# Kernel optimization log

Hardware: AMD Instinct MI355X
Metric: run time of the kernel (lower is better)

Reference implementation:

```python
import jax, jax.numpy as jnp
import numpy as np

# Static DAG: input -> L hidden layers of K nodes (dense between layers) -> output.
B, WIDTH, K, L = 262144, 64, 4, 4


def _linear_init(key, shape, fan_in):
    # matches nn.Linear default: U(-1/sqrt(fan_in), 1/sqrt(fan_in))
    bound = 1.0 / np.sqrt(fan_in)
    return jax.random.uniform(key, shape, jnp.float32, -bound, bound)


def setup_inputs() -> dict:
    key = jax.random.key(0)
    ks = jax.random.split(key, 9)
    x = jax.random.normal(ks[0], (B, WIDTH), jnp.float32)
    # input node -> first hidden layer (K edges)
    W_in = _linear_init(ks[1], (K, WIDTH, WIDTH), WIDTH)
    b_in = _linear_init(ks[2], (K, WIDTH), WIDTH)
    # between hidden layers: (L-1) transitions, K*K edges each; [pred, node, out, in]
    W_mid = _linear_init(ks[3], (L - 1, K, K, WIDTH, WIDTH), WIDTH)
    b_mid = _linear_init(ks[4], (L - 1, K, K, WIDTH), WIDTH)
    # last hidden layer -> output node (K edges)
    W_out = _linear_init(ks[5], (K, WIDTH, WIDTH), WIDTH)
    b_out = _linear_init(ks[6], (K, WIDTH), WIDTH)
    return {"x": x, "W_in": W_in, "b_in": b_in, "W_mid": W_mid,
            "b_mid": b_mid, "W_out": W_out, "b_out": b_out}


def _l2_normalize(t):
    # torch.linalg.norm(t) with no dim: Frobenius norm over the WHOLE tensor
    return t / jnp.linalg.norm(t)


def reference(x, W_in, b_in, W_mid, b_mid, W_out, b_out):
    # input node -> layer 1: each node k gets a single edge Linear, then normalize
    h = jnp.einsum('bw,kvw->kbv', x, W_in) + b_in[:, None, :]  # [K,B,W]
    h = jax.vmap(_l2_normalize)(h)
    # hidden -> hidden transitions: node v sums over its K predecessor edges
    for l in range(L - 1):  # small fixed structural loop over layers
        pre = jnp.einsum('pbw,pkvw->kbv', h, W_mid[l]) + b_mid[l].sum(axis=0)[:, None, :]
        h = jax.vmap(_l2_normalize)(pre)
    # last layer -> output node: sum K edge outputs, normalize
    out = jnp.einsum('pbw,pvw->bv', h, W_out) + b_out.sum(axis=0)
    return _l2_normalize(out)
```

## Files before the change

### kernel.cpp

```cpp
#include <hip/hip_runtime.h>


#define BF 262144.0f

#define OFF_G   0
#define OFF_S   4096
#define OFF_P0  8192
#define OFF_P1  73728
#define OFF_C0  139264
#define OFF_C1  140288
#define OFF_MO  141312
#define OFF_CO  145408

typedef __attribute__((ext_vector_type(8))) short bf16x8;
typedef __attribute__((ext_vector_type(4))) float f32x4;

__device__ __forceinline__ unsigned short f2bf(float f) {
  unsigned u = __builtin_bit_cast(unsigned, f);
  u += 0x7FFF + ((u >> 16) & 1);
  return (unsigned short)(u >> 16);
}
__device__ __forceinline__ float bf2f(unsigned short h) {
  unsigned u = ((unsigned)h) << 16;
  return __builtin_bit_cast(float, u);
}

__device__ __forceinline__ bf16x8 cvt8(f32x4 a, f32x4 b, float s) {
  bf16x8 t;
#pragma unroll
  for (int j = 0; j < 4; j++) {
    t[j]     = (short)f2bf(a[j] * s);
    t[j + 4] = (short)f2bf(b[j] * s);
  }
  return t;
}

__global__ __launch_bounds__(256) void kG(const float* __restrict__ x,
                                          float* __restrict__ Gpart) {
  __shared__ __align__(16) unsigned short xts[4][4][16][8];
  __shared__ float sred[256][4];
  const int tid = threadIdx.x;
  const int lane = tid & 63, mt = tid >> 6;
  const int col = lane & 15, q = lane >> 4;
  const int row0 = tid >> 4;
  const int cf0  = (tid & 15) * 4;

  f32x4 acc[4];
#pragma unroll
  for (int nt = 0; nt < 4; nt++) acc[nt] = (f32x4){0.f, 0.f, 0.f, 0.f};
  float s0 = 0.f, s1 = 0.f, s2 = 0.f, s3 = 0.f;

  const float* bx = x + (long)blockIdx.x * 32768;
  f32x4 r0 = *(const f32x4*)(bx + tid * 4);
  f32x4 r1 = *(const f32x4*)(bx + 1024 + tid * 4);

  for (int c = 0; c < 16; c++) {
    __syncthreads();
    s0 += r0[0] + r1[0]; s1 += r0[1] + r1[1];
    s2 += r0[2] + r1[2]; s3 += r0[3] + r1[3];
#pragma unroll
    for (int j = 0; j < 4; j++) {
      const int cf = cf0 + j;
      xts[cf >> 4][row0 >> 3][cf & 15][row0 & 7]        = f2bf(r0[j]);
      xts[cf >> 4][2 + (row0 >> 3)][cf & 15][row0 & 7]  = f2bf(r1[j]);
    }
    f32x4 r0n = r0, r1n = r1;
    if (c < 15) {
      r0n = *(const f32x4*)(bx + (c + 1) * 2048 + tid * 4);
      r1n = *(const f32x4*)(bx + (c + 1) * 2048 + 1024 + tid * 4);
    }
    __syncthreads();
    const bf16x8 af = *(const bf16x8*)xts[mt][q][col];
#pragma unroll
    for (int nt = 0; nt < 4; nt++) {
      const bf16x8 bfr = *(const bf16x8*)xts[nt][q][col];
      acc[nt] = __builtin_amdgcn_mfma_f32_16x16x32_bf16(af, bfr, acc[nt], 0, 0, 0);
    }
    r0 = r0n; r1 = r1n;
  }

  float* myp = Gpart + (long)blockIdx.x * 4160;
#pragma unroll
  for (int nt = 0; nt < 4; nt++)
#pragma unroll
    for (int r = 0; r < 4; r++)
      myp[(mt * 16 + q * 4 + r) * 64 + nt * 16 + col] = acc[nt][r];

  sred[tid][0] = s0; sred[tid][1] = s1; sred[tid][2] = s2; sred[tid][3] = s3;
  __syncthreads();
  if (tid < 64) {
    float t = 0.f;
#pragma unroll
    for (int k2 = 0; k2 < 16; k2++) t += sred[(tid >> 2) + 16 * k2][tid & 3];
    myp[4096 + tid] = t;
  }
}

__global__ __launch_bounds__(256) void kGred(const float* __restrict__ Gpart,
                                             float* __restrict__ G,
                                             float* __restrict__ s) {
  __shared__ float red[4][64];
  const int tid = threadIdx.x;
  const int e = blockIdx.x * 64 + (tid & 63);
  const int quarter = tid >> 6;
  float acc = 0.f;
#pragma unroll 4
  for (int j = 0; j < 128; j++)
    acc += Gpart[(long)(quarter * 128 + j) * 4160 + e];
  red[quarter][tid & 63] = acc;
  __syncthreads();
  if (tid < 64) {
    const float t = red[0][tid] + red[1][tid] + red[2][tid] + red[3][tid];
    const int ee = blockIdx.x * 64 + tid;
    if (ee < 4096) G[ee] = t;
    else           s[ee - 4096] = t;
  }
}

__global__ __launch_bounds__(256) void kLayer(const float* __restrict__ Tsrc,
                                              const float* __restrict__ csrc,
                                              const float* __restrict__ Wm,
                                              const float* __restrict__ bm,
                                              const float* __restrict__ G,
                                              const float* __restrict__ s,
                                              float* __restrict__ Pout,
                                              float* __restrict__ cpout,
                                              const int KN, const int first) {
  __shared__ float Tf[64][68];
  __shared__ __align__(16) unsigned short Tth[64][68], Ttl[64][68];
  __shared__ __align__(16) unsigned short Wh[64][68], Wlo[64][68];
  __shared__ float red[256];
  __shared__ __align__(16) float cl[64], sl[64];
  const int tid = threadIdx.x;
  const int p = blockIdx.x / KN, kk = blockIdx.x % KN;
  const int lane = tid & 63, it = tid >> 6;
  const int col = lane & 15, quad = lane >> 4;

  float Greg[4][4];
#pragma unroll
  for (int ut = 0; ut < 4; ut++)
#pragma unroll
    for (int r = 0; r < 4; r++)
      Greg[ut][r] = G[(it * 16 + quad * 4 + r) * 64 + ut * 16 + col];

#pragma unroll
  for (int m = 0; m < 16; m++) {
    const int li = m * 256 + tid;
    const int r = li >> 6, cc = li & 63;
    float tv;
    if (first) tv = Tsrc[p * 4096 + li];
    else tv = Tsrc[p * 4096 + li] + Tsrc[(4 + p) * 4096 + li] +
              Tsrc[(8 + p) * 4096 + li] + Tsrc[(12 + p) * 4096 + li];
    Tf[r][cc] = tv;
    const float wv = Wm[(long)(p * KN + kk) * 4096 + li];
    const unsigned short wh = f2bf(wv);
    Wh[r][cc] = wh;
    Wlo[r][cc] = f2bf(wv - bf2f(wh));
  }
  if (tid < 64) {
    float cv;
    if (first) cv = csrc[p * 64 + tid];
    else cv = csrc[p * 64 + tid] + csrc[(4 + p) * 64 + tid] +
              csrc[(8 + p) * 64 + tid] + csrc[(12 + p) * 64 + tid];
    cl[tid] = cv;
    sl[tid] = s[tid];
  }
  __syncthreads();

  {
    const int tc = tid >> 2;
    const int rb = (tid & 3) * 16;
#pragma unroll
    for (int j = 0; j < 16; j++) {
      const float tv = Tf[rb + j][tc];
      const unsigned short h = f2bf(tv);
      Tth[tc][rb + j] = h;
      Ttl[tc][rb + j] = f2bf(tv - bf2f(h));
    }
  }
  __syncthreads();

  float qp = 0.f;
  {
    f32x4 dq[4];
#pragma unroll
    for (int ut = 0; ut < 4; ut++) dq[ut] = (f32x4){0.f, 0.f, 0.f, 0.f};
#pragma unroll
    for (int ks = 0; ks < 2; ks++) {
      const bf16x8 ah = *(const bf16x8*)&Tth[it * 16 + col][ks * 32 + quad * 8];
      const bf16x8 al = *(const bf16x8*)&Ttl[it * 16 + col][ks * 32 + quad * 8];
#pragma unroll
      for (int ut = 0; ut < 4; ut++) {
        const bf16x8 bh = *(const bf16x8*)&Tth[ut * 16 + col][ks * 32 + quad * 8];
        const bf16x8 bl = *(const bf16x8*)&Ttl[ut * 16 + col][ks * 32 + quad * 8];
        dq[ut] = __builtin_amdgcn_mfma_f32_16x16x32_bf16(ah, bh, dq[ut], 0, 0, 0);
        dq[ut] = __builtin_amdgcn_mfma_f32_16x16x32_bf16(ah, bl, dq[ut], 0, 0, 0);
        dq[ut] = __builtin_amdgcn_mfma_f32_16x16x32_bf16(al, bh, dq[ut], 0, 0, 0);
      }
    }
#pragma unroll
    for (int ut = 0; ut < 4; ut++)
#pragma unroll
      for (int r = 0; r < 4; r++)
        qp += dq[ut][r] * Greg[ut][r];
  }
  if (tid < 64) {
    float sd = 0.f;
#pragma unroll
    for (int u4 = 0; u4 < 16; u4++) {
      const f32x4 tv = *(const f32x4*)&Tf[tid][u4 * 4];
      const f32x4 sv = *(const f32x4*)&sl[u4 * 4];
      sd += sv[0] * tv[0] + sv[1] * tv[1] + sv[2] * tv[2] + sv[3] * tv[3];
    }
    qp += cl[tid] * (2.f * sd + BF * cl[tid]);
  }
  red[tid] = qp;
  __syncthreads();
  for (int st = 128; st > 0; st >>= 1) {
    if (tid < st) red[tid] += red[tid + st];
    __syncthreads();
  }
  const float inv = 1.0f / sqrtf(red[0]);

  {
    f32x4 dc[4];
#pragma unroll
    for (int nt = 0; nt < 4; nt++) dc[nt] = (f32x4){0.f, 0.f, 0.f, 0.f};
#pragma unroll
    for (int ks = 0; ks < 2; ks++) {
      const bf16x8 awh = *(const bf16x8*)&Wh[it * 16 + col][ks * 32 + quad * 8];
      const bf16x8 awl = *(const bf16x8*)&Wlo[it * 16 + col][ks * 32 + quad * 8];
#pragma unroll
      for (int nt = 0; nt < 4; nt++) {
        const bf16x8 bh = *(const bf16x8*)&Tth[nt * 16 + col][ks * 32 + quad * 8];
        const bf16x8 bl = *(const bf16x8*)&Ttl[nt * 16 + col][ks * 32 + quad * 8];
        dc[nt] = __builtin_amdgcn_mfma_f32_16x16x32_bf16(awh, bh, dc[nt], 0, 0, 0);
        dc[nt] = __builtin_amdgcn_mfma_f32_16x16x32_bf16(awh, bl, dc[nt], 0, 0, 0);
        dc[nt] = __builtin_amdgcn_mfma_f32_16x16x32_bf16(awl, bh, dc[nt], 0, 0, 0);
      }
    }
    float* po = Pout + (long)(p * KN + kk) * 4096;
#pragma unroll
    for (int nt = 0; nt < 4; nt++)
#pragma unroll
      for (int r = 0; r < 4; r++)
        po[(it * 16 + quad * 4 + r) * 64 + nt * 16 + col] = inv * dc[nt][r];
  }

  if (tid < 64) {
    const float* wg = Wm + (long)(p * KN + kk) * 4096 + tid * 64;
    float pc = 0.f;
#pragma unroll
    for (int u4 = 0; u4 < 16; u4++) {
      const f32x4 wv = *(const f32x4*)(wg + u4 * 4);
      pc += wv[0] * cl[u4 * 4] + wv[1] * cl[u4 * 4 + 1] +
            wv[2] * cl[u4 * 4 + 2] + wv[3] * cl[u4 * 4 + 3];
    }
    cpout[(p * KN + kk) * 64 + tid] = inv * pc + bm[(long)(p * KN + kk) * 64 + tid];
  }
}

__global__ __launch_bounds__(256) void kNorm(const float* __restrict__ Psrc,
                                             const float* __restrict__ csrc,
                                             const float* __restrict__ G,
                                             const float* __restrict__ s,
                                             float* __restrict__ MoS,
                                             float* __restrict__ coS) {
  __shared__ float Tf[64][68];
  __shared__ __align__(16) unsigned short Tth[64][68], Ttl[64][68];
  __shared__ float red[256];
  __shared__ __align__(16) float cl[64], sl[64];
  const int tid = threadIdx.x;
  const int lane = tid & 63, it = tid >> 6;
  const int col = lane & 15, quad = lane >> 4;

  float Greg[4][4];
#pragma unroll
  for (int ut = 0; ut < 4; ut++)
#pragma unroll
    for (int r = 0; r < 4; r++)
      Greg[ut][r] = G[(it * 16 + quad * 4 + r) * 64 + ut * 16 + col];

#pragma unroll
  for (int m = 0; m < 16; m++) {
    const int li = m * 256 + tid;
    Tf[li >> 6][li & 63] = Psrc[li] + Psrc[4096 + li] + Psrc[8192 + li] + Psrc[12288 + li];
  }
  if (tid < 64) {
    cl[tid] = csrc[tid] + csrc[64 + tid] + csrc[128 + tid] + csrc[192 + tid];
    sl[tid] = s[tid];
  }
  __syncthreads();

  {
    const int tc = tid >> 2;
    const int rb = (tid & 3) * 16;
#pragma unroll
    for (int j = 0; j < 16; j++) {
      const float tv = Tf[rb + j][tc];
      const unsigned short h = f2bf(tv);
      Tth[tc][rb + j] = h;
      Ttl[tc][rb + j] = f2bf(tv - bf2f(h));
    }
  }
  __syncthreads();

  float qp = 0.f;
  {
    f32x4 dq[4];
#pragma unroll
    for (int ut = 0; ut < 4; ut++) dq[ut] = (f32x4){0.f, 0.f, 0.f, 0.f};
#pragma unroll
    for (int ks = 0; ks < 2; ks++) {
      const bf16x8 ah = *(const bf16x8*)&Tth[it * 16 + col][ks * 32 + quad * 8];
      const bf16x8 al = *(const bf16x8*)&Ttl[it * 16 + col][ks * 32 + quad * 8];
#pragma unroll
      for (int ut = 0; ut < 4; ut++) {
        const bf16x8 bh = *(const bf16x8*)&Tth[ut * 16 + col][ks * 32 + quad * 8];
        const bf16x8 bl = *(const bf16x8*)&Ttl[ut * 16 + col][ks * 32 + quad * 8];
        dq[ut] = __builtin_amdgcn_mfma_f32_16x16x32_bf16(ah, bh, dq[ut], 0, 0, 0);
        dq[ut] = __builtin_amdgcn_mfma_f32_16x16x32_bf16(ah, bl, dq[ut], 0, 0, 0);
        dq[ut] = __builtin_amdgcn_mfma_f32_16x16x32_bf16(al, bh, dq[ut], 0, 0, 0);
      }
    }
#pragma unroll
    for (int ut = 0; ut < 4; ut++)
#pragma unroll
      for (int r = 0; r < 4; r++)
        qp += dq[ut][r] * Greg[ut][r];
  }
  if (tid < 64) {
    float sd = 0.f;
#pragma unroll
    for (int u4 = 0; u4 < 16; u4++) {
      const f32x4 tv = *(const f32x4*)&Tf[tid][u4 * 4];
      const f32x4 sv = *(const f32x4*)&sl[u4 * 4];
      sd += sv[0] * tv[0] + sv[1] * tv[1] + sv[2] * tv[2] + sv[3] * tv[3];
    }
    qp += cl[tid] * (2.f * sd + BF * cl[tid]);
  }
  red[tid] = qp;
  __syncthreads();
  for (int st = 128; st > 0; st >>= 1) {
    if (tid < st) red[tid] += red[tid + st];
    __syncthreads();
  }
  const float inv = 1.0f / sqrtf(red[0]);

#pragma unroll
  for (int m = 0; m < 16; m++) {
    const int li = m * 256 + tid;
    MoS[li] = inv * Tf[li >> 6][li & 63];
  }
  if (tid < 64) coS[tid] = inv * cl[tid];
}

__global__ __launch_bounds__(256) void kApply(const float* __restrict__ x,
                                              const float* __restrict__ MoS,
                                              const float* __restrict__ coS,
                                              float* __restrict__ out) {
  const int tid = threadIdx.x, lane = tid & 63, vt = tid >> 6;
  const int col = lane & 15, q = lane >> 4;

  bf16x8 bfr[2];
  const float* mr = MoS + (vt * 16 + col) * 64 + q * 8;
  bfr[0] = cvt8(*(const f32x4*)mr, *(const f32x4*)(mr + 4), 1.f);
  bfr[1] = cvt8(*(const f32x4*)(mr + 32), *(const f32x4*)(mr + 36), 1.f);
  const float cf = coS[vt * 16 + col];

  for (int t = 0; t < 16; t++) {
    const int b0 = (blockIdx.x * 16 + t) * 16;
    const float* xr = x + (long)(b0 + col) * 64 + q * 8;
    const bf16x8 a0 = cvt8(*(const f32x4*)xr, *(const f32x4*)(xr + 4), 1.f);
    const bf16x8 a1 = cvt8(*(const f32x4*)(xr + 32), *(const f32x4*)(xr + 36), 1.f);
    f32x4 acc = (f32x4){0.f, 0.f, 0.f, 0.f};
    acc = __builtin_amdgcn_mfma_f32_16x16x32_bf16(a0, bfr[0], acc, 0, 0, 0);
    acc = __builtin_amdgcn_mfma_f32_16x16x32_bf16(a1, bfr[1], acc, 0, 0, 0);
#pragma unroll
    for (int r = 0; r < 4; r++)
      out[(long)(b0 + q * 4 + r) * 64 + vt * 16 + col] = acc[r] + cf;
  }
}

extern "C" void kernel_launch(void* const* d_in, const int* in_sizes, int n_in,
                              void* d_out, int out_size, void* d_ws, size_t ws_size,
                              hipStream_t stream) {
  const float* x    = (const float*)d_in[0];
  const float* Win  = (const float*)d_in[1];
  const float* bin  = (const float*)d_in[2];
  const float* Wmid = (const float*)d_in[3];
  const float* bmid = (const float*)d_in[4];
  const float* Wout = (const float*)d_in[5];
  const float* bout = (const float*)d_in[6];
  float* out = (float*)d_out;
  float* ws  = (float*)d_ws;
  float* Gpart = out;

  kG   <<<512, 256, 0, stream>>>(x, Gpart);
  kGred<<<65, 256, 0, stream>>>(Gpart, ws + OFF_G, ws + OFF_S);
  kLayer<<<16, 256, 0, stream>>>(Win, bin, Wmid, bmid,
                                 ws + OFF_G, ws + OFF_S, ws + OFF_P0, ws + OFF_C0, 4, 1);
  kLayer<<<16, 256, 0, stream>>>(ws + OFF_P0, ws + OFF_C0, Wmid + 65536, bmid + 1024,
                                 ws + OFF_G, ws + OFF_S, ws + OFF_P1, ws + OFF_C1, 4, 0);
  kLayer<<<16, 256, 0, stream>>>(ws + OFF_P1, ws + OFF_C1, Wmid + 131072, bmid + 2048,
                                 ws + OFF_G, ws + OFF_S, ws + OFF_P0, ws + OFF_C0, 4, 0);
  kLayer<<<4, 256, 0, stream>>>(ws + OFF_P0, ws + OFF_C0, Wout, bout,
                                 ws + OFF_G, ws + OFF_S, ws + OFF_P1, ws + OFF_C1, 1, 0);
  kNorm<<<1, 256, 0, stream>>>(ws + OFF_P1, ws + OFF_C1, ws + OFF_G, ws + OFF_S,
                               ws + OFF_MO, ws + OFF_CO);
  kApply<<<1024, 256, 0, stream>>>(x, ws + OFF_MO, ws + OFF_CO, out);
}
```

Baseline: 233.9 us.

## Fuse per-layer weight-composition kernels into one single-block chain kernel

Replaces the four kLayer launches and the kNorm launch with one single-block kernel, kChain1. It keeps the composed layer matrices in shared memory as bf16 hi/lo splits and iterates through all layers, folding each norm scale into the weights. This removes four kernel launches and the round trips of intermediates through global memory. In exchange, all composition work now runs serially on one workgroup instead of 16 blocks, so it loses parallelism and adds more block-wide syncs. Intermediate products are also now stored as bf16 hi/lo pairs rather than fp32, which may change accuracy slightly.

```diff
diff --git a/kernel.cpp b/kernel.cpp
--- a/kernel.cpp
+++ b/kernel.cpp
@@ -2,15 +2,12 @@
 
 
 #define BF 262144.0f
+#define NTW 4608
 
 #define OFF_G   0
 #define OFF_S   4096
-#define OFF_P0  8192
-#define OFF_P1  73728
-#define OFF_C0  139264
-#define OFF_C1  140288
-#define OFF_MO  141312
-#define OFF_CO  145408
+#define OFF_MO  8192
+#define OFF_CO  12288
 
 typedef __attribute__((ext_vector_type(8))) short bf16x8;
 typedef __attribute__((ext_vector_type(4))) float f32x4;
@@ -33,6 +30,34 @@
     t[j + 4] = (short)f2bf(b[j] * s);
   }
   return t;
+}
+
+__device__ __forceinline__ float qpart(const unsigned short* th,
+                                       const unsigned short* tl,
+                                       int it, int col, int quad,
+                                       const float Greg[4][4]) {
+  f32x4 dq[4];
+#pragma unroll
+  for (int ut = 0; ut < 4; ut++) dq[ut] = (f32x4){0.f, 0.f, 0.f, 0.f};
+#pragma unroll
+  for (int ks = 0; ks < 2; ks++) {
+    const bf16x8 ah = *(const bf16x8*)&th[(it * 16 + col) * 72 + ks * 32 + quad * 8];
+    const bf16x8 al = *(const bf16x8*)&tl[(it * 16 + col) * 72 + ks * 32 + quad * 8];
+#pragma unroll
+    for (int ut = 0; ut < 4; ut++) {
+      const bf16x8 bh = *(const bf16x8*)&th[(ut * 16 + col) * 72 + ks * 32 + quad * 8];
+      const bf16x8 bl = *(const bf16x8*)&tl[(ut * 16 + col) * 72 + ks * 32 + quad * 8];
+      dq[ut] = __builtin_amdgcn_mfma_f32_16x16x32_bf16(ah, bh, dq[ut], 0, 0, 0);
+      dq[ut] = __builtin_amdgcn_mfma_f32_16x16x32_bf16(ah, bl, dq[ut], 0, 0, 0);
+      dq[ut] = __builtin_amdgcn_mfma_f32_16x16x32_bf16(al, bh, dq[ut], 0, 0, 0);
+    }
+  }
+  float qp = 0.f;
+#pragma unroll
+  for (int ut = 0; ut < 4; ut++)
+#pragma unroll
+    for (int r = 0; r < 4; r++) qp += dq[ut][r] * Greg[ut][r];
+  return qp;
 }
 
 __global__ __launch_bounds__(256) void kG(const float* __restrict__ x,
@@ -117,159 +142,23 @@
   }
 }
 
-__global__ __launch_bounds__(256) void kLayer(const float* __restrict__ Tsrc,
-                                              const float* __restrict__ csrc,
-                                              const float* __restrict__ Wm,
-                                              const float* __restrict__ bm,
-                                              const float* __restrict__ G,
-                                              const float* __restrict__ s,
-                                              float* __restrict__ Pout,
-                                              float* __restrict__ cpout,
-                                              const int KN, const int first) {
-  __shared__ float Tf[64][68];
-  __shared__ __align__(16) unsigned short Tth[64][68], Ttl[64][68];
-  __shared__ __align__(16) unsigned short Wh[64][68], Wlo[64][68];
-  __shared__ float red[256];
-  __shared__ __align__(16) float cl[64], sl[64];
-  const int tid = threadIdx.x;
-  const int p = blockIdx.x / KN, kk = blockIdx.x % KN;
-  const int lane = tid & 63, it = tid >> 6;
-  const int col = lane & 15, quad = lane >> 4;
-
-  float Greg[4][4];
-#pragma unroll
-  for (int ut = 0; ut < 4; ut++)
-#pragma unroll
-    for (int r = 0; r < 4; r++)
-      Greg[ut][r] = G[(it * 16 + quad * 4 + r) * 64 + ut * 16 + col];
-
-#pragma unroll
-  for (int m = 0; m < 16; m++) {
-    const int li = m * 256 + tid;
-    const int r = li >> 6, cc = li & 63;
-    float tv;
-    if (first) tv = Tsrc[p * 4096 + li];
-    else tv = Tsrc[p * 4096 + li] + Tsrc[(4 + p) * 4096 + li] +
-              Tsrc[(8 + p) * 4096 + li] + Tsrc[(12 + p) * 4096 + li];
-    Tf[r][cc] = tv;
-    const float wv = Wm[(long)(p * KN + kk) * 4096 + li];
-    const unsigned short wh = f2bf(wv);
-    Wh[r][cc] = wh;
-    Wlo[r][cc] = f2bf(wv - bf2f(wh));
-  }
-  if (tid < 64) {
-    float cv;
-    if (first) cv = csrc[p * 64 + tid];
-    else cv = csrc[p * 64 + tid] + csrc[(4 + p) * 64 + tid] +
-              csrc[(8 + p) * 64 + tid] + csrc[(12 + p) * 64 + tid];
-    cl[tid] = cv;
-    sl[tid] = s[tid];
-  }
-  __syncthreads();
-
-  {
-    const int tc = tid >> 2;
-    const int rb = (tid & 3) * 16;
-#pragma unroll
-    for (int j = 0; j < 16; j++) {
-      const float tv = Tf[rb + j][tc];
-      const unsigned short h = f2bf(tv);
-      Tth[tc][rb + j] = h;
-      Ttl[tc][rb + j] = f2bf(tv - bf2f(h));
-    }
-  }
-  __syncthreads();
-
-  float qp = 0.f;
-  {
-    f32x4 dq[4];
-#pragma unroll
-    for (int ut = 0; ut < 4; ut++) dq[ut] = (f32x4){0.f, 0.f, 0.f, 0.f};
-#pragma unroll
-    for (int ks = 0; ks < 2; ks++) {
-      const bf16x8 ah = *(const bf16x8*)&Tth[it * 16 + col][ks * 32 + quad * 8];
-      const bf16x8 al = *(const bf16x8*)&Ttl[it * 16 + col][ks * 32 + quad * 8];
-#pragma unroll
-      for (int ut = 0; ut < 4; ut++) {
-        const bf16x8 bh = *(const bf16x8*)&Tth[ut * 16 + col][ks * 32 + quad * 8];
-        const bf16x8 bl = *(const bf16x8*)&Ttl[ut * 16 + col][ks * 32 + quad * 8];
-        dq[ut] = __builtin_amdgcn_mfma_f32_16x16x32_bf16(ah, bh, dq[ut], 0, 0, 0);
-        dq[ut] = __builtin_amdgcn_mfma_f32_16x16x32_bf16(ah, bl, dq[ut], 0, 0, 0);
-        dq[ut] = __builtin_amdgcn_mfma_f32_16x16x32_bf16(al, bh, dq[ut], 0, 0, 0);
-      }
-    }
-#pragma unroll
-    for (int ut = 0; ut < 4; ut++)
-#pragma unroll
-      for (int r = 0; r < 4; r++)
-        qp += dq[ut][r] * Greg[ut][r];
-  }
-  if (tid < 64) {
-    float sd = 0.f;
-#pragma unroll
-    for (int u4 = 0; u4 < 16; u4++) {
-      const f32x4 tv = *(const f32x4*)&Tf[tid][u4 * 4];
-      const f32x4 sv = *(const f32x4*)&sl[u4 * 4];
-      sd += sv[0] * tv[0] + sv[1] * tv[1] + sv[2] * tv[2] + sv[3] * tv[3];
-    }
-    qp += cl[tid] * (2.f * sd + BF * cl[tid]);
-  }
-  red[tid] = qp;
-  __syncthreads();
-  for (int st = 128; st > 0; st >>= 1) {
-    if (tid < st) red[tid] += red[tid + st];
-    __syncthreads();
-  }
-  const float inv = 1.0f / sqrtf(red[0]);
-
-  {
-    f32x4 dc[4];
-#pragma unroll
-    for (int nt = 0; nt < 4; nt++) dc[nt] = (f32x4){0.f, 0.f, 0.f, 0.f};
-#pragma unroll
-    for (int ks = 0; ks < 2; ks++) {
-      const bf16x8 awh = *(const bf16x8*)&Wh[it * 16 + col][ks * 32 + quad * 8];
-      const bf16x8 awl = *(const bf16x8*)&Wlo[it * 16 + col][ks * 32 + quad * 8];
-#pragma unroll
-      for (int nt = 0; nt < 4; nt++) {
-        const bf16x8 bh = *(const bf16x8*)&Tth[nt * 16 + col][ks * 32 + quad * 8];
-        const bf16x8 bl = *(const bf16x8*)&Ttl[nt * 16 + col][ks * 32 + quad * 8];
-        dc[nt] = __builtin_amdgcn_mfma_f32_16x16x32_bf16(awh, bh, dc[nt], 0, 0, 0);
-        dc[nt] = __builtin_amdgcn_mfma_f32_16x16x32_bf16(awh, bl, dc[nt], 0, 0, 0);
-        dc[nt] = __builtin_amdgcn_mfma_f32_16x16x32_bf16(awl, bh, dc[nt], 0, 0, 0);
-      }
-    }
-    float* po = Pout + (long)(p * KN + kk) * 4096;
-#pragma unroll
-    for (int nt = 0; nt < 4; nt++)
-#pragma unroll
-      for (int r = 0; r < 4; r++)
-        po[(it * 16 + quad * 4 + r) * 64 + nt * 16 + col] = inv * dc[nt][r];
-  }
-
-  if (tid < 64) {
-    const float* wg = Wm + (long)(p * KN + kk) * 4096 + tid * 64;
-    float pc = 0.f;
-#pragma unroll
-    for (int u4 = 0; u4 < 16; u4++) {
-      const f32x4 wv = *(const f32x4*)(wg + u4 * 4);
-      pc += wv[0] * cl[u4 * 4] + wv[1] * cl[u4 * 4 + 1] +
-            wv[2] * cl[u4 * 4 + 2] + wv[3] * cl[u4 * 4 + 3];
-    }
-    cpout[(p * KN + kk) * 64 + tid] = inv * pc + bm[(long)(p * KN + kk) * 64 + tid];
-  }
-}
-
-__global__ __launch_bounds__(256) void kNorm(const float* __restrict__ Psrc,
-                                             const float* __restrict__ csrc,
-                                             const float* __restrict__ G,
-                                             const float* __restrict__ s,
-                                             float* __restrict__ MoS,
-                                             float* __restrict__ coS) {
-  __shared__ float Tf[64][68];
-  __shared__ __align__(16) unsigned short Tth[64][68], Ttl[64][68];
-  __shared__ float red[256];
-  __shared__ __align__(16) float cl[64], sl[64];
+__global__ __launch_bounds__(256) void kChain1(
+    const float* __restrict__ Win, const float* __restrict__ bin,
+    const float* __restrict__ Wmid, const float* __restrict__ bmid,
+    const float* __restrict__ Wout, const float* __restrict__ bout,
+    const float* __restrict__ G, const float* __restrict__ s,
+    float* __restrict__ MoS, float* __restrict__ coS) {
+  extern __shared__ __align__(16) char smem[];
+  unsigned short* Tth = (unsigned short*)smem;
+  unsigned short* Ttl = Tth + 4 * NTW;
+  unsigned short* Wh  = Ttl + 4 * NTW;
+  unsigned short* Wlo = Wh  + 2 * NTW;
+  float* Tf   = (float*)(Wlo + 2 * NTW);
+  float* red4 = Tf + 64 * 68;
+  float* cbv  = red4 + 4;
+  float* slv  = cbv + 512;
+  float* qv   = slv + 64;
+
   const int tid = threadIdx.x;
   const int lane = tid & 63, it = tid >> 6;
   const int col = lane & 15, quad = lane >> 4;
@@ -280,79 +169,153 @@
 #pragma unroll
     for (int r = 0; r < 4; r++)
       Greg[ut][r] = G[(it * 16 + quad * 4 + r) * 64 + ut * 16 + col];
-
-#pragma unroll
-  for (int m = 0; m < 16; m++) {
-    const int li = m * 256 + tid;
-    Tf[li >> 6][li & 63] = Psrc[li] + Psrc[4096 + li] + Psrc[8192 + li] + Psrc[12288 + li];
+  if (tid < 64) slv[tid] = s[tid];
+
+  for (int p = 0; p < 4; p++) {
+#pragma unroll
+    for (int m = 0; m < 16; m++) {
+      const int li = m * 256 + tid;
+      Tf[(li >> 6) * 68 + (li & 63)] = Win[p * 4096 + li];
+    }
+    __syncthreads();
+    const int tc = tid >> 2, rb = (tid & 3) * 16;
+#pragma unroll
+    for (int j = 0; j < 16; j++) {
+      const float tv = Tf[(rb + j) * 68 + tc];
+      const unsigned short h = f2bf(tv);
+      Tth[p * NTW + tc * 72 + rb + j] = h;
+      Ttl[p * NTW + tc * 72 + rb + j] = f2bf(tv - bf2f(h));
+    }
+    __syncthreads();
   }
   if (tid < 64) {
-    cl[tid] = csrc[tid] + csrc[64 + tid] + csrc[128 + tid] + csrc[192 + tid];
-    sl[tid] = s[tid];
+#pragma unroll
+    for (int p = 0; p < 4; p++) cbv[p * 64 + tid] = bin[p * 64 + tid];
   }
   __syncthreads();
 
-  {
-    const int tc = tid >> 2;
-    const int rb = (tid & 3) * 16;
-#pragma unroll
-    for (int j = 0; j < 16; j++) {
-      const float tv = Tf[rb + j][tc];
-      const unsigned short h = f2bf(tv);
-      Tth[tc][rb + j] = h;
-      Ttl[tc][rb + j] = f2bf(tv - bf2f(h));
-    }
-  }
-  __syncthreads();
-
-  float qp = 0.f;
-  {
-    f32x4 dq[4];
-#pragma unroll
-    for (int ut = 0; ut < 4; ut++) dq[ut] = (f32x4){0.f, 0.f, 0.f, 0.f};
-#pragma unroll
-    for (int ks = 0; ks < 2; ks++) {
-      const bf16x8 ah = *(const bf16x8*)&Tth[it * 16 + col][ks * 32 + quad * 8];
-      const bf16x8 al = *(const bf16x8*)&Ttl[it * 16 + col][ks * 32 + quad * 8];
-#pragma unroll
-      for (int ut = 0; ut < 4; ut++) {
-        const bf16x8 bh = *(const bf16x8*)&Tth[ut * 16 + col][ks * 32 + quad * 8];
-        const bf16x8 bl = *(const bf16x8*)&Ttl[ut * 16 + col][ks * 32 + quad * 8];
-        dq[ut] = __builtin_amdgcn_mfma_f32_16x16x32_bf16(ah, bh, dq[ut], 0, 0, 0);
-        dq[ut] = __builtin_amdgcn_mfma_f32_16x16x32_bf16(ah, bl, dq[ut], 0, 0, 0);
-        dq[ut] = __builtin_amdgcn_mfma_f32_16x16x32_bf16(al, bh, dq[ut], 0, 0, 0);
-      }
-    }
-#pragma unroll
-    for (int ut = 0; ut < 4; ut++)
-#pragma unroll
-      for (int r = 0; r < 4; r++)
-        qp += dq[ut][r] * Greg[ut][r];
-  }
-  if (tid < 64) {
-    float sd = 0.f;
-#pragma unroll
-    for (int u4 = 0; u4 < 16; u4++) {
-      const f32x4 tv = *(const f32x4*)&Tf[tid][u4 * 4];
-      const f32x4 sv = *(const f32x4*)&sl[u4 * 4];
-      sd += sv[0] * tv[0] + sv[1] * tv[1] + sv[2] * tv[2] + sv[3] * tv[3];
-    }
-    qp += cl[tid] * (2.f * sd + BF * cl[tid]);
-  }
-  red[tid] = qp;
-  __syncthreads();
-  for (int st = 128; st > 0; st >>= 1) {
-    if (tid < st) red[tid] += red[tid + st];
-    __syncthreads();
-  }
-  const float inv = 1.0f / sqrtf(red[0]);
-
-#pragma unroll
-  for (int m = 0; m < 16; m++) {
-    const int li = m * 256 + tid;
-    MoS[li] = inv * Tf[li >> 6][li & 63];
-  }
-  if (tid < 64) coS[tid] = inv * cl[tid];
+  int cur = 0;
+  for (int lm = 0; lm < 4; lm++) {
+    const int KN = (lm < 3) ? 4 : 1;
+    const int NP = 4 * KN;
+    const float* Wb = (lm < 3) ? (Wmid + (long)lm * 65536) : Wout;
+    const float* bb = (lm < 3) ? (bmid + lm * 1024) : bout;
+
+    for (int p = 0; p < 4; p++) {
+      float qp = qpart(Tth + p * NTW, Ttl + p * NTW, it, col, quad, Greg);
+      if (tid < 64) {
+        float sd = 0.f;
+        for (int w = 0; w < 64; w++)
+          sd += slv[w] * (bf2f(Tth[p * NTW + w * 72 + tid]) +
+                          bf2f(Ttl[p * NTW + w * 72 + tid]));
+        const float c = cbv[cur * 256 + p * 64 + tid];
+        qp += c * (2.f * sd + BF * c);
+      }
+#pragma unroll
+      for (int off = 32; off; off >>= 1) qp += __shfl_down(qp, off, 64);
+      if (lane == 0) red4[it] = qp;
+      __syncthreads();
+      if (tid == 0) qv[p] = 1.0f / sqrtf(red4[0] + red4[1] + red4[2] + red4[3]);
+      __syncthreads();
+    }
+
+    f32x4 dc[4][4];
+#pragma unroll
+    for (int k = 0; k < 4; k++)
+#pragma unroll
+      for (int nt = 0; nt < 4; nt++) dc[k][nt] = (f32x4){0.f, 0.f, 0.f, 0.f};
+    float cn[4] = {0.f, 0.f, 0.f, 0.f};
+
+    f32x4 wr[4];
+#pragma unroll
+    for (int j = 0; j < 4; j++) wr[j] = *(const f32x4*)(Wb + tid * 16 + j * 4);
+
+    for (int i = 0; i < NP; i++) {
+      const int p = (KN == 4) ? (i >> 2) : i;
+      const int k = (KN == 4) ? (i & 3) : 0;
+      const int sl2 = i & 1;
+      const float invp = qv[p];
+      const int wrr = tid >> 2, wcc = (tid & 3) * 16;
+#pragma unroll
+      for (int j = 0; j < 4; j++)
+#pragma unroll
+        for (int e = 0; e < 4; e++) {
+          const float v = wr[j][e] * invp;
+          const unsigned short h = f2bf(v);
+          Wh[sl2 * NTW + wrr * 72 + wcc + j * 4 + e] = h;
+          Wlo[sl2 * NTW + wrr * 72 + wcc + j * 4 + e] = f2bf(v - bf2f(h));
+        }
+      if (i + 1 < NP) {
+#pragma unroll
+        for (int j = 0; j < 4; j++)
+          wr[j] = *(const f32x4*)(Wb + (long)(i + 1) * 4096 + tid * 16 + j * 4);
+      }
+      __syncthreads();
+#pragma unroll
+      for (int ks = 0; ks < 2; ks++) {
+        const bf16x8 awh = *(const bf16x8*)&Wh[sl2 * NTW + (it * 16 + col) * 72 + ks * 32 + quad * 8];
+        const bf16x8 awl = *(const bf16x8*)&Wlo[sl2 * NTW + (it * 16 + col) * 72 + ks * 32 + quad * 8];
+#pragma unroll
+        for (int nt = 0; nt < 4; nt++) {
+          const bf16x8 bh = *(const bf16x8*)&Tth[p * NTW + (nt * 16 + col) * 72 + ks * 32 + quad * 8];
+          const bf16x8 bl = *(const bf16x8*)&Ttl[p * NTW + (nt * 16 + col) * 72 + ks * 32 + quad * 8];
+          dc[k][nt] = __builtin_amdgcn_mfma_f32_16x16x32_bf16(awh, bh, dc[k][nt], 0, 0, 0);
+          dc[k][nt] = __builtin_amdgcn_mfma_f32_16x16x32_bf16(awh, bl, dc[k][nt], 0, 0, 0);
+          dc[k][nt] = __builtin_amdgcn_mfma_f32_16x16x32_bf16(awl, bh, dc[k][nt], 0, 0, 0);
+        }
+      }
+      if (tid < 64) {
+        float pc = 0.f;
+        for (int u = 0; u < 64; u++)
+          pc += cbv[cur * 256 + p * 64 + u] *
+                (bf2f(Wh[sl2 * NTW + tid * 72 + u]) + bf2f(Wlo[sl2 * NTW + tid * 72 + u]));
+        cn[k] += pc + bb[i * 64 + tid];
+      }
+    }
+    __syncthreads();
+
+    for (int k = 0; k < KN; k++) {
+#pragma unroll
+      for (int nt = 0; nt < 4; nt++)
+#pragma unroll
+        for (int r = 0; r < 4; r++) {
+          const float val = dc[k][nt][r];
+          const unsigned short h = f2bf(val);
+          const int w_ = nt * 16 + col, v_ = it * 16 + quad * 4 + r;
+          Tth[k * NTW + w_ * 72 + v_] = h;
+          Ttl[k * NTW + w_ * 72 + v_] = f2bf(val - bf2f(h));
+        }
+    }
+    if (tid < 64) {
+      for (int k = 0; k < KN; k++) cbv[(cur ^ 1) * 256 + k * 64 + tid] = cn[k];
+    }
+    __syncthreads();
+
+    if (lm == 3) {
+      float qp = qpart(Tth, Ttl, it, col, quad, Greg);
+      if (tid < 64) {
+        float sd = 0.f;
+        for (int w = 0; w < 64; w++)
+          sd += slv[w] * (bf2f(Tth[w * 72 + tid]) + bf2f(Ttl[w * 72 + tid]));
+        const float c = cbv[(cur ^ 1) * 256 + tid];
+        qp += c * (2.f * sd + BF * c);
+      }
+#pragma unroll
+      for (int off = 32; off; off >>= 1) qp += __shfl_down(qp, off, 64);
+      if (lane == 0) red4[it] = qp;
+      __syncthreads();
+      if (tid == 0) qv[0] = 1.0f / sqrtf(red4[0] + red4[1] + red4[2] + red4[3]);
+      __syncthreads();
+      const float invo = qv[0];
+#pragma unroll
+      for (int nt = 0; nt < 4; nt++)
+#pragma unroll
+        for (int r = 0; r < 4; r++)
+          MoS[(it * 16 + quad * 4 + r) * 64 + nt * 16 + col] = invo * dc[0][nt][r];
+      if (tid < 64) coS[tid] = invo * cbv[(cur ^ 1) * 256 + tid];
+    }
+    cur ^= 1;
+  }
 }
 
 __global__ __launch_bounds__(256) void kApply(const float* __restrict__ x,
@@ -396,17 +359,15 @@
   float* ws  = (float*)d_ws;
   float* Gpart = out;
 
+  const size_t SMEM = (size_t)(12 * NTW) * 2 +
+                      (size_t)(64 * 68 + 4 + 512 + 64 + 4) * 4;
+  hipFuncSetAttribute((const void*)kChain1,
+                      hipFuncAttributeMaxDynamicSharedMemorySize, (int)SMEM);
+
   kG   <<<512, 256, 0, stream>>>(x, Gpart);
   kGred<<<65, 256, 0, stream>>>(Gpart, ws + OFF_G, ws + OFF_S);
-  kLayer<<<16, 256, 0, stream>>>(Win, bin, Wmid, bmid,
-                                 ws + OFF_G, ws + OFF_S, ws + OFF_P0, ws + OFF_C0, 4, 1);
-  kLayer<<<16, 256, 0, stream>>>(ws + OFF_P0, ws + OFF_C0, Wmid + 65536, bmid + 1024,
-                                 ws + OFF_G, ws + OFF_S, ws + OFF_P1, ws + OFF_C1, 4, 0);
-  kLayer<<<16, 256, 0, stream>>>(ws + OFF_P1, ws + OFF_C1, Wmid + 131072, bmid + 2048,
-                                 ws + OFF_G, ws + OFF_S, ws + OFF_P0, ws + OFF_C0, 4, 0);
-  kLayer<<<4, 256, 0, stream>>>(ws + OFF_P0, ws + OFF_C0, Wout, bout,
-                                 ws + OFF_G, ws + OFF_S, ws + OFF_P1, ws + OFF_C1, 1, 0);
-  kNorm<<<1, 256, 0, stream>>>(ws + OFF_P1, ws + OFF_C1, ws + OFF_G, ws + OFF_S,
-                               ws + OFF_MO, ws + OFF_CO);
+  kChain1<<<1, 256, SMEM, stream>>>(Win, bin, Wmid, bmid, Wout, bout,
+                                    ws + OFF_G, ws + OFF_S,
+                                    ws + OFF_MO, ws + OFF_CO);
   kApply<<<1024, 256, 0, stream>>>(x, ws + OFF_MO, ws + OFF_CO, out);
 }
```

Result: slower. 384.9 us (+64.5%).
